# Kernel tuning notes

Measured on AMD Instinct MI355X. Metric: run time of the kernel, lower is better.

Reference implementation:

```python
import jax, jax.numpy as jnp
import numpy as np

N_HEADS = 4
NUM_GROUPS = 32
EPS = 1e-6


def _nin(t, W, b):
    # 1x1 conv as dense over channel dim: [B,C,H,W] x [C,D] -> [B,D,H,W]
    return jnp.einsum('bchw,cd->bdhw', t, W) + b[None, :, None, None]


def setup_inputs() -> dict:
    key = jax.random.key(0)
    ks = jax.random.split(key, 12)
    B, C, H, W = 8, 256, 32, 32
    Tc = 512
    Cin = C + Tc  # 768
    x = jax.random.normal(ks[0], (B, C, H, W), dtype=jnp.float32)
    text_feat = jax.random.normal(ks[1], (B, Tc), dtype=jnp.float32)
    gn_gamma = jnp.ones((Cin,), dtype=jnp.float32)
    gn_beta = jnp.zeros((Cin,), dtype=jnp.float32)
    scale = 1.0 / np.sqrt(Cin)
    W0 = jax.random.normal(ks[2], (Cin, C), dtype=jnp.float32) * scale
    b0 = jnp.zeros((C,), dtype=jnp.float32)
    W1 = jax.random.normal(ks[3], (Cin, C), dtype=jnp.float32) * scale
    b1 = jnp.zeros((C,), dtype=jnp.float32)
    W2 = jax.random.normal(ks[4], (Cin, C), dtype=jnp.float32) * scale
    b2 = jnp.zeros((C,), dtype=jnp.float32)
    return {"x": x, "text_feat": text_feat, "gn_gamma": gn_gamma, "gn_beta": gn_beta,
            "W0": W0, "b0": b0, "W1": W1, "b1": b1, "W2": W2, "b2": b2}


def reference(x, text_feat, gn_gamma, gn_beta, W0, b0, W1, b1, W2, b2):
    B, C, H, W = x.shape
    # broadcast text features spatially and concat on channel dim
    tf = jnp.broadcast_to(text_feat[:, :, None, None], (B, text_feat.shape[1], H, W))
    h = jnp.concatenate([x, tf], axis=1)  # [B, C+Tc, H, W]
    Ctot = h.shape[1]
    # GroupNorm(32, Ctot), eps=1e-6
    hg = h.reshape(B, NUM_GROUPS, Ctot // NUM_GROUPS, H, W)
    mu = hg.mean(axis=(2, 3, 4), keepdims=True)
    var = hg.var(axis=(2, 3, 4), keepdims=True)
    hn = ((hg - mu) * jax.lax.rsqrt(var + EPS)).reshape(B, Ctot, H, W)
    hn = hn * gn_gamma[None, :, None, None] + gn_beta[None, :, None, None]
    q = _nin(hn, W0, b0)
    k = _nin(hn, W1, b1)
    v = _nin(hn, W2, b2)
    Ch = C // N_HEADS
    qh = q.reshape(B * N_HEADS, Ch, H, W)
    kh = k.reshape(B * N_HEADS, Ch, H, W)
    vh = v.reshape(B * N_HEADS, Ch, H, W)
    # full HW x HW attention scores, softmax over flattened key positions
    w = jnp.einsum('bchw,bcij->bhwij', qh, kh) * (Ch ** -0.5)
    w = jax.nn.softmax(w.reshape(B * N_HEADS, H, W, H * W), axis=-1)
    w = w.reshape(B * N_HEADS, H, W, H, W)
    ho = jnp.einsum('bhwij,bcij->bchw', w, vh).reshape(B, C, H, W)
    return x + ho
```

## Files before the change

### kernel.cpp

```cpp
#include <hip/hip_runtime.h>
#include <math.h>

#define BATCH 8
#define CX 256
#define TC 512
#define CIN 768
#define HW_TOT 1024
#define NH 4
#define CHD 64

typedef __attribute__((ext_vector_type(8))) short short8;
typedef __attribute__((ext_vector_type(4))) short s4v;
typedef __attribute__((ext_vector_type(4))) float floatx4;

static __device__ __forceinline__ short f2bf(float f) {
    union { float f; unsigned u; } c; c.f = f;
    unsigned r = (c.u + 0x7fffu + ((c.u >> 16) & 1u)) >> 16;
    return (short)r;
}

__global__ __launch_bounds__(256)
void gn_part_kernel(const float* __restrict__ x,
                    float* __restrict__ psum, float* __restrict__ psumsq) {
    const int t = threadIdx.x;
    const int row = blockIdx.x * 4 + (t >> 6);
    const int lane = t & 63;
    const float4* p = (const float4*)(x + (size_t)row * HW_TOT);
    float s = 0.f, ss = 0.f;
    #pragma unroll
    for (int i = 0; i < 4; i++) {
        float4 v = p[lane + 64 * i];
        s += v.x + v.y + v.z + v.w;
        ss += v.x * v.x + v.y * v.y + v.z * v.z + v.w * v.w;
    }
    #pragma unroll
    for (int d = 1; d < 64; d <<= 1) {
        s += __shfl_xor(s, d);
        ss += __shfl_xor(ss, d);
    }
    if (lane == 0) { psum[row] = s; psumsq[row] = ss; }
}

__global__ __launch_bounds__(64)
void gn_fin_kernel(const float* __restrict__ psum, const float* __restrict__ psumsq,
                   const float* __restrict__ tf,
                   const float* __restrict__ gamma, const float* __restrict__ beta,
                   float* __restrict__ scale, float* __restrict__ shift) {
    const int b = blockIdx.x >> 5;
    const int g = blockIdx.x & 31;
    const int lane = threadIdx.x;
    const int cg = g * 24 + lane;
    float s = 0.f, ss = 0.f;
    if (lane < 24) {
        if (cg < CX) {
            s = psum[b * CX + cg];
            ss = psumsq[b * CX + cg];
        } else {
            float v = tf[b * TC + cg - CX];
            s = 1024.f * v;
            ss = 1024.f * v * v;
        }
    }
    #pragma unroll
    for (int d = 1; d < 64; d <<= 1) {
        s += __shfl_xor(s, d);
        ss += __shfl_xor(ss, d);
    }
    const float inv_n = 1.f / (24 * 1024);
    float mean = s * inv_n;
    float var = ss * inv_n - mean * mean;
    float rs = rsqrtf(var + 1e-6f);
    if (lane < 24) {
        float sc = gamma[cg] * rs;
        scale[b * CIN + cg] = sc;
        shift[b * CIN + cg] = beta[cg] - mean * sc;
    }
}

__global__ __launch_bounds__(256)
void prep_kernel(const float* __restrict__ x, const float* __restrict__ tf,
                 const float* __restrict__ scale, const float* __restrict__ shift,
                 const float* __restrict__ W0, const float* __restrict__ W1,
                 const float* __restrict__ W2,
                 short* __restrict__ hnT, short* __restrict__ Wt,
                 float* __restrict__ tc) {
    __shared__ float hs[TC];
    __shared__ float red[4][64];
    const int bx = blockIdx.x;
    const int t = threadIdx.x;
    if (bx < 256) {
        int id = (bx & 31) * 256 + t;
        int b = id >> 10;
        const float* xb = x + (size_t)b * CX * HW_TOT + (id & 1023);
        const float* scb = scale + b * CIN;
        const float* shb = shift + b * CIN;
        short* outp = hnT + (size_t)id * CX;
        int c0base = (bx >> 5) * 32;
        for (int c0 = c0base; c0 < c0base + 32; c0 += 8) {
            short8 o;
            #pragma unroll
            for (int i = 0; i < 8; i++) {
                float v = xb[(size_t)(c0 + i) * HW_TOT];
                o[i] = f2bf(v * scb[c0 + i] + shb[c0 + i]);
            }
            *(short8*)(outp + c0) = o;
        }
    } else if (bx < 268) {
        int m = bx - 256;
        int dg = (m % 3) * 256 + t;
        int which = dg >> 8, d = dg & 255;
        const float* Wm = (which == 0) ? W0 : (which == 1) ? W1 : W2;
        int c0base = (m / 3) * 64;
        for (int c0 = c0base; c0 < c0base + 64; c0 += 8) {
            short8 o;
            #pragma unroll
            for (int i = 0; i < 8; i++) o[i] = f2bf(Wm[(size_t)(c0 + i) * CX + d]);
            *(short8*)(Wt + (size_t)dg * CX + c0) = o;
        }
    } else {
        int m = bx - 268;
        int b = m & 7, dt = m >> 3;
        int which = dt >> 2, d0 = (dt & 3) * 64;
        const float* Wm = (which == 0) ? W0 : (which == 1) ? W1 : W2;
        for (int c = t; c < TC; c += 256)
            hs[c] = tf[b * TC + c] * scale[b * CIN + CX + c] + shift[b * CIN + CX + c];
        __syncthreads();
        int td = t & 63, tq = t >> 6;
        float acc = 0.f;
        const float* wp = Wm + (size_t)(CX + tq * 128) * CX + d0 + td;
        for (int c = 0; c < 128; c++)
            acc = fmaf(hs[tq * 128 + c], wp[(size_t)c * CX], acc);
        red[tq][td] = acc;
        __syncthreads();
        if (t < 64)
            tc[b * CIN + which * CX + d0 + t] = red[0][t] + red[1][t] + red[2][t] + red[3][t];
    }
}

__global__ __launch_bounds__(256)
void qkv_gemm(const short* __restrict__ hnT, const short* __restrict__ Wt,
              const float* __restrict__ tc,
              const float* __restrict__ b0, const float* __restrict__ b1,
              const float* __restrict__ b2,
              short* __restrict__ qb, short* __restrict__ kb, short* __restrict__ vb) {
    const int hw0 = blockIdx.x * 128, dt = blockIdx.y, b = blockIdx.z;
    const int dg0 = dt * 128;
    const int which = dt >> 1;
    const bool OV = (which == 2);

    __shared__ short At[128 * 40];
    __shared__ short Bt[128 * 40];

    const int t = threadIdx.x;
    const int w = t >> 6, l = t & 63;
    const int wm = w >> 1, wn = w & 1;
    const int l15 = l & 15, q = l >> 4;

    const int srow = t >> 1, sch = (t & 1) * 16;
    const short* gA = hnT + (size_t)(b * HW_TOT + hw0 + srow) * CX + sch;
    const short* gB = Wt + (size_t)(dg0 + srow) * CX + sch;
    short* lA = At + srow * 40 + sch;
    short* lB = Bt + srow * 40 + sch;

    floatx4 acc[4][4] = {};
    for (int k0 = 0; k0 < CX; k0 += 32) {
        __syncthreads();
        *(short8*)lA       = *(const short8*)(gA + k0);
        *(short8*)(lA + 8) = *(const short8*)(gA + k0 + 8);
        *(short8*)lB       = *(const short8*)(gB + k0);
        *(short8*)(lB + 8) = *(const short8*)(gB + k0 + 8);
        __syncthreads();
        const short* aBase = OV ? Bt : At;
        const short* bBase = OV ? At : Bt;
        short8 af[4], bf[4];
        #pragma unroll
        for (int mt = 0; mt < 4; mt++)
            af[mt] = *(const short8*)(aBase + (wm * 64 + mt * 16 + l15) * 40 + q * 8);
        #pragma unroll
        for (int nt = 0; nt < 4; nt++)
            bf[nt] = *(const short8*)(bBase + (wn * 64 + nt * 16 + l15) * 40 + q * 8);
        #pragma unroll
        for (int mt = 0; mt < 4; mt++)
            #pragma unroll
            for (int nt = 0; nt < 4; nt++)
                acc[mt][nt] = __builtin_amdgcn_mfma_f32_16x16x32_bf16(
                    af[mt], bf[nt], acc[mt][nt], 0, 0, 0);
    }

    __syncthreads();
    const float* bias = (which == 0) ? b0 : (which == 1) ? b1 : b2;
    short* epi = At + w * (16 * 72);

    float colAdd[4];
    if (!OV) {
        #pragma unroll
        for (int nt = 0; nt < 4; nt++) {
            int cl = (dt & 1) * 128 + wn * 64 + l15 + nt * 16;
            colAdd[nt] = bias[cl] + tc[b * CIN + which * CX + cl];
        }
    }
    const int row_l = l >> 2, ch = l & 3;
    #pragma unroll
    for (int mt = 0; mt < 4; mt++) {
        #pragma unroll
        for (int rr = 0; rr < 4; rr++) {
            float radd = 0.f;
            if (OV) {
                int rl = (dt & 1) * 128 + wm * 64 + mt * 16 + q * 4 + rr;
                radd = bias[rl] + tc[b * CIN + 2 * CX + rl];
            }
            #pragma unroll
            for (int nt = 0; nt < 4; nt++) {
                float val = acc[mt][nt][rr] + (OV ? radd : colAdd[nt]);
                epi[(q * 4 + rr) * 72 + l15 + nt * 16] = f2bf(val);
            }
        }
        short8 v0 = *(const short8*)(epi + row_l * 72 + ch * 16);
        short8 v1 = *(const short8*)(epi + row_l * 72 + ch * 16 + 8);
        if (!OV) {
            short* outp = (which == 0) ? qb : kb;
            size_t off = (size_t)(b * HW_TOT + hw0 + wm * 64 + mt * 16 + row_l) * CX
                       + (dt & 1) * 128 + wn * 64 + ch * 16;
            *(short8*)(outp + off) = v0;
            *(short8*)(outp + off + 8) = v1;
        } else {
            size_t off = (size_t)(b * CX + (dt & 1) * 128 + wm * 64 + mt * 16 + row_l) * HW_TOT
                       + hw0 + wn * 64 + ch * 16;
            *(short8*)(vb + off) = v0;
            *(short8*)(vb + off + 8) = v1;
        }
    }
}

__global__ __launch_bounds__(256)
void attn_part(const short* __restrict__ qb, const short* __restrict__ kb,
               const short* __restrict__ vb,
               float* __restrict__ opart, float* __restrict__ lpart) {
    const int qt = blockIdx.x, bh = blockIdx.y, sp = blockIdx.z;
    const int b = bh >> 2, h = bh & 3;
    const int hw0 = qt * 64;

    __shared__ short Qs[64 * 72];
    __shared__ short Ks[64 * 72];
    __shared__ short Vs[64 * 72];

    const int t = threadIdx.x;
    const int w = t >> 6, l = t & 63;
    const int l15 = l & 15, q = l >> 4;
    const int srow = t >> 2, sch = (t & 3) * 16;

    {
        const short* gq = qb + (size_t)(b * HW_TOT + hw0 + srow) * CX + h * CHD + sch;
        *(short8*)(Qs + srow * 72 + sch)     = *(const short8*)gq;
        *(short8*)(Qs + srow * 72 + sch + 8) = *(const short8*)(gq + 8);
    }

    short8 pk0, pk1, pv0, pv1;
    {
        const int j0 = sp * 512;
        const short* gk = kb + (size_t)(b * HW_TOT + j0 + srow) * CX + h * CHD + sch;
        pk0 = *(const short8*)gk;
        pk1 = *(const short8*)(gk + 8);
        const short* gv = vb + (size_t)(b * CX + h * CHD + srow) * HW_TOT + j0 + sch;
        pv0 = *(const short8*)gv;
        pv1 = *(const short8*)(gv + 8);
    }
    __syncthreads();
    const short8 aq0 = *(const short8*)(Qs + (w * 16 + l15) * 72 + q * 8);
    const short8 aq1 = *(const short8*)(Qs + (w * 16 + l15) * 72 + 32 + q * 8);

    floatx4 oacc[4] = {};
    float lsum = 0.f;

    for (int jj = 0; jj < 8; jj++) {
        *(short8*)(Ks + srow * 72 + sch)     = pk0;
        *(short8*)(Ks + srow * 72 + sch + 8) = pk1;
        *(short8*)(Vs + srow * 72 + sch)     = pv0;
        *(short8*)(Vs + srow * 72 + sch + 8) = pv1;
        __syncthreads();

        if (jj < 7) {
            const int j0 = sp * 512 + (jj + 1) * 64;
            const short* gk = kb + (size_t)(b * HW_TOT + j0 + srow) * CX + h * CHD + sch;
            pk0 = *(const short8*)gk;
            pk1 = *(const short8*)(gk + 8);
            const short* gv = vb + (size_t)(b * CX + h * CHD + srow) * HW_TOT + j0 + sch;
            pv0 = *(const short8*)gv;
            pv1 = *(const short8*)(gv + 8);
        }

        floatx4 sacc[4] = {};
        #pragma unroll
        for (int nt = 0; nt < 4; nt++) {
            short8 kf0 = *(const short8*)(Ks + (nt * 16 + l15) * 72 + q * 8);
            short8 kf1 = *(const short8*)(Ks + (nt * 16 + l15) * 72 + 32 + q * 8);
            sacc[nt] = __builtin_amdgcn_mfma_f32_16x16x32_bf16(kf0, aq0, sacc[nt], 0, 0, 0);
            sacc[nt] = __builtin_amdgcn_mfma_f32_16x16x32_bf16(kf1, aq1, sacc[nt], 0, 0, 0);
        }

        short8 pf[2];
        #pragma unroll
        for (int nt = 0; nt < 4; nt++)
            #pragma unroll
            for (int r = 0; r < 4; r++) {
                float e = __expf(fmaf(sacc[nt][r], 0.125f, -10.f));
                lsum += e;
                pf[nt >> 1][(nt & 1) * 4 + r] = f2bf(e);
            }

        #pragma unroll
        for (int ct = 0; ct < 4; ct++) {
            const short* vr = Vs + (ct * 16 + l15) * 72;
            #pragma unroll
            for (int kcc = 0; kcc < 2; kcc++) {
                s4v vlo = *(const s4v*)(vr + kcc * 32 + q * 4);
                s4v vhi = *(const s4v*)(vr + kcc * 32 + 16 + q * 4);
                short8 vf = __builtin_shufflevector(vlo, vhi, 0, 1, 2, 3, 4, 5, 6, 7);
                oacc[ct] = __builtin_amdgcn_mfma_f32_16x16x32_bf16(vf, pf[kcc], oacc[ct], 0, 0, 0);
            }
        }
        __syncthreads();
    }

    float* op = opart + ((size_t)(sp * BATCH + b) * CX) * HW_TOT;
    #pragma unroll
    for (int ct = 0; ct < 4; ct++)
        #pragma unroll
        for (int r = 0; r < 4; r++) {
            int c = h * CHD + ct * 16 + q * 4 + r;
            op[(size_t)c * HW_TOT + hw0 + w * 16 + l15] = oacc[ct][r];
        }
    lsum += __shfl_xor(lsum, 16);
    lsum += __shfl_xor(lsum, 32);
    if (q == 0)
        lpart[(size_t)(sp * 32 + bh) * HW_TOT + hw0 + w * 16 + l15] = lsum;
}

__global__ __launch_bounds__(256)
void attn_epi(const float* __restrict__ opart, const float* __restrict__ lpart,
              const float* __restrict__ x, float* __restrict__ out) {
    const int idx = (blockIdx.x * 256 + threadIdx.x) * 4;
    const int b = idx >> 18, c = (idx >> 10) & 255, hw = idx & 1023;
    const int bh = b * 4 + (c >> 6);
    const size_t lo = (size_t)bh * HW_TOT + hw;
    float4 l0 = *(const float4*)(lpart + lo);
    float4 l1 = *(const float4*)(lpart + 32 * HW_TOT + lo);
    float4 o0 = *(const float4*)(opart + idx);
    float4 o1 = *(const float4*)(opart + BATCH * CX * HW_TOT + idx);
    float4 xv = *(const float4*)(x + idx);
    float4 ov;
    ov.x = xv.x + (o0.x + o1.x) / (l0.x + l1.x);
    ov.y = xv.y + (o0.y + o1.y) / (l0.y + l1.y);
    ov.z = xv.z + (o0.z + o1.z) / (l0.z + l1.z);
    ov.w = xv.w + (o0.w + o1.w) / (l0.w + l1.w);
    *(float4*)(out + idx) = ov;
}

extern "C" void kernel_launch(void* const* d_in, const int* in_sizes, int n_in,
                              void* d_out, int out_size, void* d_ws, size_t ws_size,
                              hipStream_t stream) {
    (void)in_sizes; (void)n_in; (void)out_size; (void)ws_size;
    const float* x     = (const float*)d_in[0];
    const float* tf    = (const float*)d_in[1];
    const float* gamma = (const float*)d_in[2];
    const float* beta  = (const float*)d_in[3];
    const float* W0 = (const float*)d_in[4];
    const float* b0 = (const float*)d_in[5];
    const float* W1 = (const float*)d_in[6];
    const float* b1 = (const float*)d_in[7];
    const float* W2 = (const float*)d_in[8];
    const float* b2 = (const float*)d_in[9];

    char* ws = (char*)d_ws;
    float* scale  = (float*)(ws);
    float* shift  = (float*)(ws + 24576);
    float* tcb    = (float*)(ws + 49152);
    short* Wt     = (short*)(ws + 73728);
    short* hnT    = (short*)(ws + 466944);
    short* qb     = (short*)(ws + 4661248);
    short* kb     = (short*)(ws + 8855552);
    short* vb     = (short*)(ws + 13049856);
    float* psum   = (float*)(ws + 17244160);
    float* psumsq = (float*)(ws + 17252352);
    float* opart  = (float*)(ws + 17260544);
    float* lpart  = (float*)(ws + 34037760);

    hipLaunchKernelGGL(gn_part_kernel, dim3(512), dim3(256), 0, stream, x, psum, psumsq);
    hipLaunchKernelGGL(gn_fin_kernel, dim3(256), dim3(64), 0, stream,
                       psum, psumsq, tf, gamma, beta, scale, shift);
    hipLaunchKernelGGL(prep_kernel, dim3(364), dim3(256), 0, stream,
                       x, tf, scale, shift, W0, W1, W2, hnT, Wt, tcb);
    hipLaunchKernelGGL(qkv_gemm, dim3(8, 6, BATCH), dim3(256), 0, stream,
                       hnT, Wt, tcb, b0, b1, b2, qb, kb, vb);
    hipLaunchKernelGGL(attn_part, dim3(16, 32, 2), dim3(256), 0, stream,
                       qb, kb, vb, opart, lpart);
    hipLaunchKernelGGL(attn_epi, dim3(2048), dim3(256), 0, stream,
                       opart, lpart, x, (float*)d_out);
}
```

Before: 128.2 us.

## Fuse GroupNorm stats into one kernel and merge split-K attention epilogue via atomic counter

Merges the two GroupNorm kernels into one that computes per-group statistics directly with an in-block reduction. Removes the separate attention epilogue kernel: each split writes its partial output, and whichever of the two split blocks finishes second (found through an atomic counter) combines both partials, normalises and adds the residual. This cuts two launches and one full pass over the partial buffers, at the cost of threadfence/atomic synchronisation and uncoalesced output writes in the combining block. The counters are reset inside the GroupNorm kernel on every call.

New measurement: 300.5 us. 2.34x slower.

```diff
diff --git a/kernel.cpp b/kernel.cpp
--- a/kernel.cpp
+++ b/kernel.cpp
@@ -20,58 +20,52 @@
 }
 
 __global__ __launch_bounds__(256)
-void gn_part_kernel(const float* __restrict__ x,
-                    float* __restrict__ psum, float* __restrict__ psumsq) {
+void gn_kernel(const float* __restrict__ x, const float* __restrict__ tf,
+               const float* __restrict__ gamma, const float* __restrict__ beta,
+               float* __restrict__ scale, float* __restrict__ shift,
+               unsigned* __restrict__ cnt) {
+    const int b = blockIdx.x >> 5;
+    const int g = blockIdx.x & 31;
     const int t = threadIdx.x;
-    const int row = blockIdx.x * 4 + (t >> 6);
-    const int lane = t & 63;
-    const float4* p = (const float4*)(x + (size_t)row * HW_TOT);
+    const int w = t >> 6, lane = t & 63;
+    if (t < 2) cnt[blockIdx.x * 2 + t] = 0u;
+
     float s = 0.f, ss = 0.f;
     #pragma unroll
-    for (int i = 0; i < 4; i++) {
-        float4 v = p[lane + 64 * i];
-        s += v.x + v.y + v.z + v.w;
-        ss += v.x * v.x + v.y * v.y + v.z * v.z + v.w * v.w;
+    for (int rr = 0; rr < 6; rr++) {
+        const int row = w * 6 + rr;
+        const int cg = g * 24 + row;
+        if (cg < CX) {
+            const float4* p = (const float4*)(x + ((size_t)b * CX + cg) * HW_TOT);
+            #pragma unroll
+            for (int i = 0; i < 4; i++) {
+                float4 v = p[lane + 64 * i];
+                s += v.x + v.y + v.z + v.w;
+                ss += v.x * v.x + v.y * v.y + v.z * v.z + v.w * v.w;
+            }
+        } else {
+            float v = tf[b * TC + cg - CX];
+            s += 16.f * v;
+            ss += 16.f * v * v;
+        }
     }
     #pragma unroll
     for (int d = 1; d < 64; d <<= 1) {
         s += __shfl_xor(s, d);
         ss += __shfl_xor(ss, d);
     }
-    if (lane == 0) { psum[row] = s; psumsq[row] = ss; }
-}
-
-__global__ __launch_bounds__(64)
-void gn_fin_kernel(const float* __restrict__ psum, const float* __restrict__ psumsq,
-                   const float* __restrict__ tf,
-                   const float* __restrict__ gamma, const float* __restrict__ beta,
-                   float* __restrict__ scale, float* __restrict__ shift) {
-    const int b = blockIdx.x >> 5;
-    const int g = blockIdx.x & 31;
-    const int lane = threadIdx.x;
-    const int cg = g * 24 + lane;
-    float s = 0.f, ss = 0.f;
-    if (lane < 24) {
-        if (cg < CX) {
-            s = psum[b * CX + cg];
-            ss = psumsq[b * CX + cg];
-        } else {
-            float v = tf[b * TC + cg - CX];
-            s = 1024.f * v;
-            ss = 1024.f * v * v;
-        }
-    }
-    #pragma unroll
-    for (int d = 1; d < 64; d <<= 1) {
-        s += __shfl_xor(s, d);
-        ss += __shfl_xor(ss, d);
-    }
+    __shared__ float rs_[4], rss_[4];
+    if (lane == 0) { rs_[w] = s; rss_[w] = ss; }
+    __syncthreads();
+    const float S  = rs_[0] + rs_[1] + rs_[2] + rs_[3];
+    const float SS = rss_[0] + rss_[1] + rss_[2] + rss_[3];
     const float inv_n = 1.f / (24 * 1024);
-    float mean = s * inv_n;
-    float var = ss * inv_n - mean * mean;
-    float rs = rsqrtf(var + 1e-6f);
-    if (lane < 24) {
-        float sc = gamma[cg] * rs;
+    const float mean = S * inv_n;
+    const float var = SS * inv_n - mean * mean;
+    const float r = rsqrtf(var + 1e-6f);
+    if (t < 24) {
+        int cg = g * 24 + t;
+        float sc = gamma[cg] * r;
         scale[b * CIN + cg] = sc;
         shift[b * CIN + cg] = beta[cg] - mean * sc;
     }
@@ -233,9 +227,10 @@
 }
 
 __global__ __launch_bounds__(256)
-void attn_part(const short* __restrict__ qb, const short* __restrict__ kb,
-               const short* __restrict__ vb,
-               float* __restrict__ opart, float* __restrict__ lpart) {
+void attn_kernel(const short* __restrict__ qb, const short* __restrict__ kb,
+                 const short* __restrict__ vb, const float* __restrict__ x,
+                 float* __restrict__ opart, float* __restrict__ lpart,
+                 unsigned* __restrict__ cnt, float* __restrict__ out) {
     const int qt = blockIdx.x, bh = blockIdx.y, sp = blockIdx.z;
     const int b = bh >> 2, h = bh & 3;
     const int hw0 = qt * 64;
@@ -243,6 +238,7 @@
     __shared__ short Qs[64 * 72];
     __shared__ short Ks[64 * 72];
     __shared__ short Vs[64 * 72];
+    __shared__ unsigned oldv;
 
     const int t = threadIdx.x;
     const int w = t >> 6, l = t & 63;
@@ -322,6 +318,9 @@
         __syncthreads();
     }
 
+    lsum += __shfl_xor(lsum, 16);
+    lsum += __shfl_xor(lsum, 32);
+
     float* op = opart + ((size_t)(sp * BATCH + b) * CX) * HW_TOT;
     #pragma unroll
     for (int ct = 0; ct < 4; ct++)
@@ -330,30 +329,28 @@
             int c = h * CHD + ct * 16 + q * 4 + r;
             op[(size_t)c * HW_TOT + hw0 + w * 16 + l15] = oacc[ct][r];
         }
-    lsum += __shfl_xor(lsum, 16);
-    lsum += __shfl_xor(lsum, 32);
     if (q == 0)
         lpart[(size_t)(sp * 32 + bh) * HW_TOT + hw0 + w * 16 + l15] = lsum;
-}
-
-__global__ __launch_bounds__(256)
-void attn_epi(const float* __restrict__ opart, const float* __restrict__ lpart,
-              const float* __restrict__ x, float* __restrict__ out) {
-    const int idx = (blockIdx.x * 256 + threadIdx.x) * 4;
-    const int b = idx >> 18, c = (idx >> 10) & 255, hw = idx & 1023;
-    const int bh = b * 4 + (c >> 6);
-    const size_t lo = (size_t)bh * HW_TOT + hw;
-    float4 l0 = *(const float4*)(lpart + lo);
-    float4 l1 = *(const float4*)(lpart + 32 * HW_TOT + lo);
-    float4 o0 = *(const float4*)(opart + idx);
-    float4 o1 = *(const float4*)(opart + BATCH * CX * HW_TOT + idx);
-    float4 xv = *(const float4*)(x + idx);
-    float4 ov;
-    ov.x = xv.x + (o0.x + o1.x) / (l0.x + l1.x);
-    ov.y = xv.y + (o0.y + o1.y) / (l0.y + l1.y);
-    ov.z = xv.z + (o0.z + o1.z) / (l0.z + l1.z);
-    ov.w = xv.w + (o0.w + o1.w) / (l0.w + l1.w);
-    *(float4*)(out + idx) = ov;
+
+    __threadfence();
+    __syncthreads();
+    if (t == 0) oldv = atomicAdd(&cnt[qt * 32 + bh], 1u);
+    __syncthreads();
+    if (oldv == 0) return;
+
+    __threadfence();
+    const int osp = 1 - sp;
+    const float* oo = opart + ((size_t)(osp * BATCH + b) * CX) * HW_TOT;
+    const float lo = lpart[(size_t)(osp * 32 + bh) * HW_TOT + hw0 + w * 16 + l15];
+    const float rinv = 1.f / (lsum + lo);
+    #pragma unroll
+    for (int ct = 0; ct < 4; ct++)
+        #pragma unroll
+        for (int r = 0; r < 4; r++) {
+            int c = h * CHD + ct * 16 + q * 4 + r;
+            size_t idx = (size_t)(b * CX + c) * HW_TOT + hw0 + w * 16 + l15;
+            out[idx] = x[idx] + (oacc[ct][r] + oo[(size_t)c * HW_TOT + hw0 + w * 16 + l15]) * rinv;
+        }
 }
 
 extern "C" void kernel_launch(void* const* d_in, const int* in_sizes, int n_in,
@@ -380,20 +377,16 @@
     short* qb     = (short*)(ws + 4661248);
     short* kb     = (short*)(ws + 8855552);
     short* vb     = (short*)(ws + 13049856);
-    float* psum   = (float*)(ws + 17244160);
-    float* psumsq = (float*)(ws + 17252352);
-    float* opart  = (float*)(ws + 17260544);
-    float* lpart  = (float*)(ws + 34037760);
-
-    hipLaunchKernelGGL(gn_part_kernel, dim3(512), dim3(256), 0, stream, x, psum, psumsq);
-    hipLaunchKernelGGL(gn_fin_kernel, dim3(256), dim3(64), 0, stream,
-                       psum, psumsq, tf, gamma, beta, scale, shift);
+    float* opart  = (float*)(ws + 17244160);
+    float* lpart  = (float*)(ws + 34021376);
+    unsigned* cnt = (unsigned*)(ws + 34283520);
+
+    hipLaunchKernelGGL(gn_kernel, dim3(256), dim3(256), 0, stream,
+                       x, tf, gamma, beta, scale, shift, cnt);
     hipLaunchKernelGGL(prep_kernel, dim3(364), dim3(256), 0, stream,
                        x, tf, scale, shift, W0, W1, W2, hnT, Wt, tcb);
     hipLaunchKernelGGL(qkv_gemm, dim3(8, 6, BATCH), dim3(256), 0, stream,
                        hnT, Wt, tcb, b0, b1, b2, qb, kb, vb);
-    hipLaunchKernelGGL(attn_part, dim3(16, 32, 2), dim3(256), 0, stream,
-                       qb, kb, vb, opart, lpart);
-    hipLaunchKernelGGL(attn_epi, dim3(2048), dim3(256), 0, stream,
-                       opart, lpart, x, (float*)d_out);
-}
+    hipLaunchKernelGGL(attn_kernel, dim3(16, 32, 2), dim3(256), 0, stream,
+                       qb, kb, vb, x, opart, lpart, cnt, (float*)d_out);
+}
```
